# Kernel tuning notes

Measured on AMD Instinct MI355X. Metric: run time of the kernel, lower is better.

## Reference

```python
import jax, jax.numpy as jnp
import numpy as np

N = 16384          # batch of signals
DIM_T = 256        # time steps per signal
DT = 0.01          # integration dt (intg_lev=1 -> dt_intg = dt)
NUF = 256          # num_units_feat
HID_XI = 128       # hidlayers_xi
HID_AUX = 64       # hidlayers_aux1_dec
LEN_INTG = DIM_T   # (dim_t-1)*intg_lev + 1 with intg_lev=1


def _linear_init(key, fan_in, fan_out):
    # torch nn.Linear default: U(-1/sqrt(fan_in), 1/sqrt(fan_in))
    s = 1.0 / np.sqrt(fan_in)
    kw, kb = jax.random.split(key)
    W = jax.random.uniform(kw, (fan_in, fan_out), minval=-s, maxval=s, dtype=jnp.float32)
    b = jax.random.uniform(kb, (fan_out,), minval=-s, maxval=s, dtype=jnp.float32)
    return W, b


def setup_inputs() -> dict:
    key = jax.random.key(0)
    ks = jax.random.split(key, 12)
    data = jax.random.normal(ks[0], (N, DIM_T), dtype=jnp.float32)
    omega = jax.random.normal(ks[1], (N, 1), dtype=jnp.float32)
    eps = jax.random.normal(ks[2], (N, 1), dtype=jnp.float32)
    # feature extractor (mlp branch): [dim_t+1 -> 256 -> 256], relu after both (actfun_output=True)
    W_feat1, b_feat1 = _linear_init(ks[3], DIM_T + 1, NUF)
    W_feat2, b_feat2 = _linear_init(ks[4], NUF, NUF)
    # xi mean head: MLP [256 -> 128 -> 1] then Softplus
    W_xim1, b_xim1 = _linear_init(ks[5], NUF, HID_XI)
    W_xim2, b_xim2 = _linear_init(ks[6], HID_XI, 1)
    # xi lnvar head: MLP [256 -> 128 -> 1]
    W_xil1, b_xil1 = _linear_init(ks[7], NUF, HID_XI)
    W_xil2, b_xil2 = _linear_init(ks[8], HID_XI, 1)
    # decoder aux1 MLP: [dim_z_aux1+1=2 -> 64 -> 1]
    W_aux1, b_aux1 = _linear_init(ks[9], 2, HID_AUX)
    W_aux2, b_aux2 = _linear_init(ks[10], HID_AUX, 1)
    return dict(data=data, omega=omega, eps=eps,
                W_feat1=W_feat1, b_feat1=b_feat1, W_feat2=W_feat2, b_feat2=b_feat2,
                W_xim1=W_xim1, b_xim1=b_xim1, W_xim2=W_xim2, b_xim2=b_xim2,
                W_xil1=W_xil1, b_xil1=b_xil1, W_xil2=W_xil2, b_xil2=b_xil2,
                W_aux1=W_aux1, b_aux1=b_aux1, W_aux2=W_aux2, b_aux2=b_aux2)


def reference(data, omega, eps,
              W_feat1, b_feat1, W_feat2, b_feat2,
              W_xim1, b_xim1, W_xim2, b_xim2,
              W_xil1, b_xil1, W_xil2, b_xil2,
              W_aux1, b_aux1, W_aux2, b_aux2):
    relu = jax.nn.relu
    # ---- encode_xi ----
    x_ = jnp.concatenate([data, omega], axis=1)                 # [n, dim_t+1]
    feat = relu(relu(x_ @ W_feat1 + b_feat1) @ W_feat2 + b_feat2)  # [n, 256]
    xi_mean = jax.nn.softplus(relu(feat @ W_xim1 + b_xim1) @ W_xim2 + b_xim2)  # [n, 1]
    xi_lnvar = relu(feat @ W_xil1 + b_xil1) @ W_xil2 + b_xil2                  # [n, 1]
    # ---- draw (reparameterization + clamp to feasible range [0, 1]) ----
    xi = xi_mean + jnp.exp(0.5 * xi_lnvar) * eps
    xi = jnp.clip(xi, 0.0, 1.0)
    # ---- decode: Euler odeint over LEN_INTG steps of state yy=[y, dy/dt] ----
    init_y = data[:, :1]                                        # [n, 1]
    initcond = jnp.concatenate([init_y, jnp.zeros_like(init_y)], axis=1)  # [n, 2]

    def step(yy, _):
        # physics: d[y, v]/dt = [v, 0]; aux MLP adds acceleration from (z_aux1=omega, y)
        aux_in = jnp.concatenate([omega, yy[:, :1]], axis=1)    # [n, 2]
        acc = relu(aux_in @ W_aux1 + b_aux1) @ W_aux2 + b_aux2  # [n, 1]
        dyy = jnp.concatenate([yy[:, 1:2], acc], axis=1)        # [n, 2]
        return yy + DT * dyy, yy

    _, yy_seq = jax.lax.scan(step, initcond, None, length=LEN_INTG)  # [len_intg, n, 2]
    y_seq = yy_seq[:, :, 0].T                                   # [n, dim_t] (intg_lev=1)
    t_intg = DT * jnp.arange(LEN_INTG, dtype=jnp.float32)       # [dim_t]
    x_PAB = jnp.exp(-jnp.abs(xi) * t_intg[None, :]) * y_seq     # [n, dim_t]
    return xi_mean, xi_lnvar, x_PAB
```

## Files before the change

kernel.cpp:

```cpp
#include <hip/hip_runtime.h>
#include <math.h>

#define NROWS 16384
#define DT_C 0.01f

typedef short s16x8 __attribute__((ext_vector_type(8)));
typedef float f32x4 __attribute__((ext_vector_type(4)));
typedef float f32x2 __attribute__((ext_vector_type(2)));

__device__ __forceinline__ unsigned short f2bf(float f) {
    unsigned u = __float_as_uint(f);
    u += 0x7fffu + ((u >> 16) & 1u);
    return (unsigned short)(u >> 16);
}
__device__ __forceinline__ unsigned pack2bf(float a, float b) {
    return (unsigned)f2bf(a) | ((unsigned)f2bf(b) << 16);
}
template <int CTRL>
__device__ __forceinline__ float dppadd(float v) {
    int x = __builtin_amdgcn_update_dpp(0, __float_as_int(v), CTRL, 0xF, 0xF, true);
    return v + __int_as_float(x);
}
__device__ __forceinline__ float sum8(float p) {
    p = dppadd<0xB1>(p);
    p = dppadd<0x4E>(p);
    p = dppadd<0x141>(p);
    return p;
}

__global__ __launch_bounds__(256) void prep_k(
    const float* __restrict__ Wf1, const float* __restrict__ Wf2,
    const float* __restrict__ Wm1, const float* __restrict__ Wl1,
    const float* __restrict__ bm1, const float* __restrict__ bl1,
    unsigned short* __restrict__ wpack, float* __restrict__ biasH)
{
    const int id = blockIdx.x * 256 + threadIdx.x;
    const int n  = id & 255;
    const int k8 = (id >> 8) & 31;
    const int s  = id >> 13;

    unsigned short tmp[8];
    #pragma unroll
    for (int j = 0; j < 8; ++j) {
        const int k = k8 * 8 + j;
        float v;
        if (s == 0)      v = Wf1[k * 256 + n];
        else if (s == 1) v = Wf2[k * 256 + n];
        else             v = (n < 128) ? Wm1[k * 128 + n] : Wl1[k * 128 + n - 128];
        tmp[j] = f2bf(v);
    }
    *(uint4*)&wpack[((s * 32 + k8) * 256 + n) * 8] = *(const uint4*)tmp;

    if (id < 256) biasH[id] = (id < 128) ? bm1[id] : bl1[id - 128];
}

__global__ __launch_bounds__(256, 2) void fused_k(
    const float* __restrict__ data, const float* __restrict__ omega,
    const float* __restrict__ eps_g,
    const unsigned short* __restrict__ wpack, const float* __restrict__ biasH,
    const float* __restrict__ bf1, const float* __restrict__ bf2,
    const float* __restrict__ w256g,
    const float* __restrict__ Wm2, const float* __restrict__ bm2,
    const float* __restrict__ Wl2, const float* __restrict__ bl2,
    const float* __restrict__ Wa1, const float* __restrict__ ba1,
    const float* __restrict__ Wa2, const float* __restrict__ ba2,
    float* __restrict__ out_mean, float* __restrict__ out_lnvar,
    float* __restrict__ xout)
{
    __shared__ __align__(16) unsigned char smem[33024];
    unsigned short* As1 = (unsigned short*)smem;
    unsigned short* Hs  = (unsigned short*)(smem + 16384);
    float* headsF = (float*)smem;
    float* omg = (float*)(smem + 32768);
    float* xiS = omg + 32;

    const int tid  = threadIdx.x;
    const int wid  = tid >> 6;
    const int lane = tid & 63;
    const int ln   = lane & 15;
    const int quad = lane >> 4;
    const int r0   = blockIdx.x * 32;

    {
        #pragma unroll
        for (int g2 = 0; g2 < 8; ++g2) {
            const int unit = g2 * 256 + tid;
            const int m    = unit >> 6;
            const int c16  = unit & 63;
            const int kblk = c16 >> 1;
            const int h    = c16 & 1;
            const float4 v = *(const float4*)&data[(size_t)(r0 + m) * 256 + c16 * 4];
            unsigned* d = (unsigned*)&As1[((kblk * 32) + (m ^ (kblk & 7))) * 8 + h * 4];
            d[0] = pack2bf(v.x, v.y);
            d[1] = pack2bf(v.z, v.w);
        }
        if (tid < 32) omg[tid] = omega[r0 + tid];
    }
    __syncthreads();

    {
        const int r   = tid >> 3;
        const int l   = tid & 7;
        const int row = r0 + r;
        const float om = omg[r];
        const float pseed = ba2[0] * 0.125f;

        f32x2 w1v[4], Av[4], w2v[4];
        #pragma unroll
        for (int i = 0; i < 4; ++i) {
            const f32x2 w0 = *(const f32x2*)&Wa1[l * 8 + i * 2];
            const f32x2 bb = *(const f32x2*)&ba1[l * 8 + i * 2];
            w1v[i] = *(const f32x2*)&Wa1[64 + l * 8 + i * 2];
            w2v[i] = *(const f32x2*)&Wa2[l * 8 + i * 2];
            Av[i]  = f32x2{fmaf(om, w0.x, bb.x), fmaf(om, w0.y, bb.y)};
        }

        auto partial = [&](float y) -> float {
            const f32x2 y2 = f32x2{y, y};
            f32x2 acc2 = f32x2{pseed, 0.f};
            #pragma unroll
            for (int i = 0; i < 4; ++i) {
                f32x2 h = __builtin_elementwise_fma(y2, w1v[i], Av[i]);
                h = __builtin_elementwise_max(h, f32x2{0.f, 0.f});
                acc2 = __builtin_elementwise_fma(h, w2v[i], acc2);
            }
            return acc2.x + acc2.y;
        };

        const float y0 = data[(size_t)row * 256];
        float ym = y0;
        float yc = y0;
        const float DT2 = DT_C * DT_C;
        float pr = sum8(partial(ym));

        float* orow = xout + (size_t)row * 256 + l * 4;
        for (int tb = 0; tb < 8; ++tb) {
            float cur[4];
            #pragma unroll
            for (int j = 0; j < 32; ++j) {
                if ((j >> 2) == l) cur[j & 3] = ym;
                float pn = sum8(partial(yc));
                const float ynext = fmaf(DT2, pr, fmaf(2.f, yc, -ym));
                ym = yc; yc = ynext; pr = pn;
            }
            *(float4*)&orow[tb * 32] = *(const float4*)cur;
        }
    }

    f32x4 acc[2][4];

    auto seed = [&](const float* bias) {
        #pragma unroll
        for (int nt = 0; nt < 4; ++nt) {
            const float b = bias[wid * 64 + nt * 16 + ln];
            acc[0][nt] = f32x4{b, b, b, b};
            acc[1][nt] = acc[0][nt];
        }
    };

    auto run_stage = [&](const unsigned short* Ap, const unsigned short* wp) {
        #pragma unroll
        for (int c = 0; c < 4; ++c) {
            #pragma unroll
            for (int kk = 0; kk < 2; ++kk) {
                const int kb   = kk * 4 + quad;
                const int kblk = c * 8 + kb;
                const int f    = kblk & 7;
                s16x8 b0 = *(const s16x8*)&wp[((size_t)(kblk * 256) + wid * 64 + 0 * 16 + ln) * 8];
                s16x8 b1 = *(const s16x8*)&wp[((size_t)(kblk * 256) + wid * 64 + 1 * 16 + ln) * 8];
                s16x8 b2 = *(const s16x8*)&wp[((size_t)(kblk * 256) + wid * 64 + 2 * 16 + ln) * 8];
                s16x8 b3 = *(const s16x8*)&wp[((size_t)(kblk * 256) + wid * 64 + 3 * 16 + ln) * 8];
                s16x8 a0 = *(const s16x8*)&Ap[(kblk * 32 + (ln ^ f)) * 8];
                s16x8 a1 = *(const s16x8*)&Ap[(kblk * 32 + ((ln ^ f) + 16)) * 8];
                acc[0][0] = __builtin_amdgcn_mfma_f32_16x16x32_bf16(a0, b0, acc[0][0], 0, 0, 0);
                acc[1][0] = __builtin_amdgcn_mfma_f32_16x16x32_bf16(a1, b0, acc[1][0], 0, 0, 0);
                acc[0][1] = __builtin_amdgcn_mfma_f32_16x16x32_bf16(a0, b1, acc[0][1], 0, 0, 0);
                acc[1][1] = __builtin_amdgcn_mfma_f32_16x16x32_bf16(a1, b1, acc[1][1], 0, 0, 0);
                acc[0][2] = __builtin_amdgcn_mfma_f32_16x16x32_bf16(a0, b2, acc[0][2], 0, 0, 0);
                acc[1][2] = __builtin_amdgcn_mfma_f32_16x16x32_bf16(a1, b2, acc[1][2], 0, 0, 0);
                acc[0][3] = __builtin_amdgcn_mfma_f32_16x16x32_bf16(a0, b3, acc[0][3], 0, 0, 0);
                acc[1][3] = __builtin_amdgcn_mfma_f32_16x16x32_bf16(a1, b3, acc[1][3], 0, 0, 0);
            }
        }
    };

    auto write_packed = [&](unsigned short* dst, bool addOm) {
        #pragma unroll
        for (int nt = 0; nt < 4; ++nt) {
            const int col = wid * 64 + nt * 16 + ln;
            const int kg  = col >> 3, f = kg & 7, jj = col & 7;
            const float wo = addOm ? w256g[col] : 0.f;
            #pragma unroll
            for (int mt = 0; mt < 2; ++mt) {
                #pragma unroll
                for (int r = 0; r < 4; ++r) {
                    const int row = mt * 16 + quad * 4 + r;
                    float v = acc[mt][nt][r];
                    if (addOm) v = fmaf(omg[row], wo, v);
                    v = fmaxf(v, 0.f);
                    dst[(kg * 32 + (row ^ f)) * 8 + jj] = f2bf(v);
                }
            }
        }
    };

    seed(bf1);
    run_stage(As1, wpack);
    write_packed(Hs, true);
    __syncthreads();
    seed(bf2);
    run_stage(Hs, wpack + 65536);
    write_packed(As1, false);
    __syncthreads();
    seed(biasH);
    run_stage(As1, wpack + 131072);
    __syncthreads();
    #pragma unroll
    for (int nt = 0; nt < 4; ++nt) {
        const int col = wid * 64 + nt * 16 + ln;
        #pragma unroll
        for (int mt = 0; mt < 2; ++mt) {
            #pragma unroll
            for (int r = 0; r < 4; ++r) {
                const int row = mt * 16 + quad * 4 + r;
                headsF[row * 256 + ((col + row * 8) & 255)] = fmaxf(acc[mt][nt][r], 0.f);
            }
        }
    }
    __syncthreads();

    {
        const int m = tid >> 3, l = tid & 7;
        float pm = 0.f, pl = 0.f;
        #pragma unroll
        for (int q = 0; q < 4; ++q) {
            const int c0 = l * 16 + q * 4;
            const float4 hm = *(const float4*)&headsF[m * 256 + ((c0 + m * 8) & 255)];
            const float4 wm = *(const float4*)&Wm2[c0];
            const float4 hl = *(const float4*)&headsF[m * 256 + ((128 + c0 + m * 8) & 255)];
            const float4 wl = *(const float4*)&Wl2[c0];
            pm = fmaf(hm.w, wm.w, fmaf(hm.z, wm.z, fmaf(hm.y, wm.y, fmaf(hm.x, wm.x, pm))));
            pl = fmaf(hl.w, wl.w, fmaf(hl.z, wl.z, fmaf(hl.y, wl.y, fmaf(hl.x, wl.x, pl))));
        }
        pm = sum8(pm);
        pl = sum8(pl);
        if (l == 0) {
            const float xm  = pm + bm2[0];
            const float mean = fmaxf(xm, 0.f) + log1pf(expf(-fabsf(xm)));
            const float lnv  = pl + bl2[0];
            out_mean[r0 + m]  = mean;
            out_lnvar[r0 + m] = lnv;
            float xi = mean + expf(0.5f * lnv) * eps_g[r0 + m];
            xiS[m] = fminf(fmaxf(xi, 0.f), 1.f);
        }
    }
    __syncthreads();

    {
        const int r   = tid >> 3;
        const int l   = tid & 7;
        const float nxdt = -xiS[r] * DT_C;
        float* orow = xout + (size_t)(r0 + r) * 256 + l * 4;
        #pragma unroll
        for (int tb = 0; tb < 8; ++tb) {
            float4 v = *(const float4*)&orow[tb * 32];
            const int c0 = tb * 32 + l * 4;
            v.x *= __expf(nxdt * (float)(c0 + 0));
            v.y *= __expf(nxdt * (float)(c0 + 1));
            v.z *= __expf(nxdt * (float)(c0 + 2));
            v.w *= __expf(nxdt * (float)(c0 + 3));
            *(float4*)&orow[tb * 32] = v;
        }
    }
}

extern "C" void kernel_launch(void* const* d_in, const int* in_sizes, int n_in,
                              void* d_out, int out_size, void* d_ws, size_t ws_size,
                              hipStream_t stream)
{
    const float* data    = (const float*)d_in[0];
    const float* omega   = (const float*)d_in[1];
    const float* eps     = (const float*)d_in[2];
    const float* W_feat1 = (const float*)d_in[3];
    const float* b_feat1 = (const float*)d_in[4];
    const float* W_feat2 = (const float*)d_in[5];
    const float* b_feat2 = (const float*)d_in[6];
    const float* W_xim1  = (const float*)d_in[7];
    const float* b_xim1  = (const float*)d_in[8];
    const float* W_xim2  = (const float*)d_in[9];
    const float* b_xim2  = (const float*)d_in[10];
    const float* W_xil1  = (const float*)d_in[11];
    const float* b_xil1  = (const float*)d_in[12];
    const float* W_xil2  = (const float*)d_in[13];
    const float* b_xil2  = (const float*)d_in[14];
    const float* W_aux1  = (const float*)d_in[15];
    const float* b_aux1  = (const float*)d_in[16];
    const float* W_aux2  = (const float*)d_in[17];
    const float* b_aux2  = (const float*)d_in[18];

    float* out_mean  = (float*)d_out;
    float* out_lnvar = out_mean + NROWS;
    float* out_x     = out_lnvar + NROWS;

    unsigned short* wpack = (unsigned short*)d_ws;
    float* biasH = (float*)((char*)d_ws + 3 * 32 * 256 * 8 * 2);

    prep_k<<<96, 256, 0, stream>>>(W_feat1, W_feat2, W_xim1, W_xil1,
                                   b_xim1, b_xil1, wpack, biasH);
    fused_k<<<512, 256, 0, stream>>>(data, omega, eps, wpack, biasH,
                                     b_feat1, b_feat2, W_feat1 + 256 * 256,
                                     W_xim2, b_xim2, W_xil2, b_xil2,
                                     W_aux1, b_aux1, W_aux2, b_aux2,
                                     out_mean, out_lnvar, out_x);
}
```

Baseline: 141.1 us.

## Replace per-step aux MLP with piecewise-linear segment tracking over sorted ReLU breakpoints

The 64-unit ReLU aux MLP is a piecewise-linear function of y for a fixed omega. The new code precomputes the breakpoints -a/w per row, sorts them with a rank count in shared memory, and stores per-segment slope and intercept deltas. The Euler loop, run by one thread per row, then evaluates acc as segB*y+segA and walks across segments as y crosses breakpoints. It also fuses the exp(-xi t) decay into the integration loop, using a running multiplicative factor instead of a second read-modify-write pass. The cost is a serial loop in one thread of eight per row, more shared memory that may reduce occupancy, and edge-case handling for ties and w=0 breakpoints.

```diff
diff --git a/kernel.cpp b/kernel.cpp
--- a/kernel.cpp
+++ b/kernel.cpp
@@ -7,6 +7,8 @@
 typedef short s16x8 __attribute__((ext_vector_type(8)));
 typedef float f32x4 __attribute__((ext_vector_type(4)));
 typedef float f32x2 __attribute__((ext_vector_type(2)));
+typedef unsigned long long u64;
+typedef unsigned long long u64x2 __attribute__((ext_vector_type(2)));
 
 __device__ __forceinline__ unsigned short f2bf(float f) {
     unsigned u = __float_as_uint(f);
@@ -26,6 +28,10 @@
     p = dppadd<0x4E>(p);
     p = dppadd<0x141>(p);
     return p;
+}
+__device__ __forceinline__ unsigned ordf(float f) {
+    unsigned u = __float_as_uint(f);
+    return u ^ ((unsigned)((int)u >> 31) | 0x80000000u);
 }
 
 __global__ __launch_bounds__(256) void prep_k(
@@ -67,12 +73,15 @@
     float* __restrict__ out_mean, float* __restrict__ out_lnvar,
     float* __restrict__ xout)
 {
-    __shared__ __align__(16) unsigned char smem[33024];
+    __shared__ __align__(16) unsigned char smem[59136];
     unsigned short* As1 = (unsigned short*)smem;
     unsigned short* Hs  = (unsigned short*)(smem + 16384);
     float* headsF = (float*)smem;
     float* omg = (float*)(smem + 32768);
     float* xiS = omg + 32;
+    float* tS  = (float*)(smem + 33024);
+    float* dP  = (float*)(smem + 41728);
+    u64*  keyU = (u64*)(smem + 41728);
 
     const int tid  = threadIdx.x;
     const int wid  = tid >> 6;
@@ -96,54 +105,63 @@
         }
         if (tid < 32) omg[tid] = omega[r0 + tid];
     }
-    __syncthreads();
-
+
+    const int sr = tid >> 3;
+    const int sl = tid & 7;
+    float tA[8], dAv[8], dBv[8];
+    u64 key[8];
+    float k0f, Af, Bf, y0_s;
     {
-        const int r   = tid >> 3;
-        const int l   = tid & 7;
-        const int row = r0 + r;
-        const float om = omg[r];
-        const float pseed = ba2[0] * 0.125f;
-
-        f32x2 w1v[4], Av[4], w2v[4];
-        #pragma unroll
-        for (int i = 0; i < 4; ++i) {
-            const f32x2 w0 = *(const f32x2*)&Wa1[l * 8 + i * 2];
-            const f32x2 bb = *(const f32x2*)&ba1[l * 8 + i * 2];
-            w1v[i] = *(const f32x2*)&Wa1[64 + l * 8 + i * 2];
-            w2v[i] = *(const f32x2*)&Wa2[l * 8 + i * 2];
-            Av[i]  = f32x2{fmaf(om, w0.x, bb.x), fmaf(om, w0.y, bb.y)};
-        }
-
-        auto partial = [&](float y) -> float {
-            const f32x2 y2 = f32x2{y, y};
-            f32x2 acc2 = f32x2{pseed, 0.f};
+        const float om_s = omega[r0 + sr];
+        y0_s = data[(size_t)(r0 + sr) * 256];
+        const u64 ky0 = ((u64)ordf(y0_s)) << 6;
+        float k0p = 0.f, Ap = 0.f, Bp = 0.f;
+        #pragma unroll
+        for (int m = 0; m < 8; ++m) {
+            const int i = sl * 8 + m;
+            const float a = fmaf(om_s, Wa1[i], ba1[i]);
+            const float w = Wa1[64 + i];
+            const float c = Wa2[i];
+            const float ca = c * a, cw = c * w;
+            const bool wpos = w > 0.f;
+            tA[m]  = -a / w;
+            dAv[m] = wpos ? ca : -ca;
+            dBv[m] = wpos ? cw : -cw;
+            key[m] = (((u64)ordf(tA[m])) << 6) | (u64)i;
+            const bool crossed = key[m] < ky0;
+            if (wpos == crossed) { Ap += ca; Bp += cw; }
+            k0p += crossed ? 1.f : 0.f;
+            keyU[sr * 64 + i] = key[m];
+        }
+        k0f = sum8(k0p);
+        Af  = sum8(Ap) + ba2[0];
+        Bf  = sum8(Bp);
+    }
+    __syncthreads();
+
+    {
+        int rk[8] = {0, 0, 0, 0, 0, 0, 0, 0};
+        const u64* krow = keyU + sr * 64;
+        for (int j = 0; j < 64; j += 2) {
+            const u64x2 kk = *(const u64x2*)&krow[j];
             #pragma unroll
-            for (int i = 0; i < 4; ++i) {
-                f32x2 h = __builtin_elementwise_fma(y2, w1v[i], Av[i]);
-                h = __builtin_elementwise_max(h, f32x2{0.f, 0.f});
-                acc2 = __builtin_elementwise_fma(h, w2v[i], acc2);
-            }
-            return acc2.x + acc2.y;
-        };
-
-        const float y0 = data[(size_t)row * 256];
-        float ym = y0;
-        float yc = y0;
-        const float DT2 = DT_C * DT_C;
-        float pr = sum8(partial(ym));
-
-        float* orow = xout + (size_t)row * 256 + l * 4;
-        for (int tb = 0; tb < 8; ++tb) {
-            float cur[4];
-            #pragma unroll
-            for (int j = 0; j < 32; ++j) {
-                if ((j >> 2) == l) cur[j & 3] = ym;
-                float pn = sum8(partial(yc));
-                const float ynext = fmaf(DT2, pr, fmaf(2.f, yc, -ym));
-                ym = yc; yc = ynext; pr = pn;
-            }
-            *(float4*)&orow[tb * 32] = *(const float4*)cur;
+            for (int m = 0; m < 8; ++m)
+                rk[m] += (int)(kk.x < key[m]) + (int)(kk.y < key[m]);
+        }
+        __syncthreads();
+        #pragma unroll
+        for (int m = 0; m < 8; ++m) {
+            const int idx = sr * 68 + 2 + rk[m];
+            tS[idx] = tA[m];
+            *(f32x2*)&dP[2 * idx] = f32x2{dAv[m], dBv[m]};
+        }
+        if (sl == 0) {
+            const int b = sr * 68;
+            const float INFV = __builtin_inff();
+            tS[b] = -INFV; tS[b + 1] = -INFV; tS[b + 66] = INFV; tS[b + 67] = INFV;
+            const f32x2 z = {0.f, 0.f};
+            *(f32x2*)&dP[2 * b] = z;          *(f32x2*)&dP[2 * (b + 1)] = z;
+            *(f32x2*)&dP[2 * (b + 66)] = z;   *(f32x2*)&dP[2 * (b + 67)] = z;
         }
     }
 
@@ -256,20 +274,53 @@
     }
     __syncthreads();
 
-    {
-        const int r   = tid >> 3;
-        const int l   = tid & 7;
-        const float nxdt = -xiS[r] * DT_C;
-        float* orow = xout + (size_t)(r0 + r) * 256 + l * 4;
-        #pragma unroll
-        for (int tb = 0; tb < 8; ++tb) {
-            float4 v = *(const float4*)&orow[tb * 32];
-            const int c0 = tb * 32 + l * 4;
-            v.x *= __expf(nxdt * (float)(c0 + 0));
-            v.y *= __expf(nxdt * (float)(c0 + 1));
-            v.z *= __expf(nxdt * (float)(c0 + 2));
-            v.w *= __expf(nxdt * (float)(c0 + 3));
-            *(float4*)&orow[tb * 32] = v;
+    if (sl == 0) {
+        const float xi   = xiS[sr];
+        const float dfac = expf(-xi * DT_C);
+        const float* tSr = tS + sr * 68 + 2;
+        const float* dPb = dP + (sr * 68 + 2) * 2;
+        int   k    = (int)k0f;
+        float segA = Af, segB = Bf;
+        float tLo  = tSr[k - 1], tHi = tSr[k], tHi2 = tSr[k + 1], tLo2 = tSr[k - 2];
+        f32x2 dU = *(const f32x2*)&dPb[2 * k];
+        f32x2 dD = *(const f32x2*)&dPb[2 * (k - 1)];
+        float ym = y0_s, yc = y0_s;
+        float pr = fmaf(segB, y0_s, segA);
+        float d  = 1.f;
+        const float DT2 = DT_C * DT_C;
+        float* orow = xout + (size_t)(r0 + sr) * 256;
+
+        auto step = [&](float& dst) {
+            if (__builtin_expect(yc >= tHi, 0)) {
+                do {
+                    segA += dU.x; segB += dU.y;
+                    dD = dU;
+                    tLo2 = tLo; tLo = tHi; tHi = tHi2;
+                    ++k;
+                    tHi2 = tSr[k + 1];
+                    dU = *(const f32x2*)&dPb[2 * k];
+                } while (yc >= tHi);
+            } else if (__builtin_expect(yc < tLo, 0)) {
+                do {
+                    segA -= dD.x; segB -= dD.y;
+                    dU = dD;
+                    tHi2 = tHi; tHi = tLo; tLo = tLo2;
+                    --k;
+                    tLo2 = tSr[k - 2];
+                    dD = *(const f32x2*)&dPb[2 * (k - 1)];
+                } while (yc < tLo);
+            }
+            const float pn = fmaf(segB, yc, segA);
+            dst = ym * d;
+            d *= dfac;
+            const float yn = fmaf(DT2, pr, fmaf(2.f, yc, -ym));
+            ym = yc; yc = yn; pr = pn;
+        };
+
+        for (int g = 0; g < 64; ++g) {
+            float4 cv;
+            step(cv.x); step(cv.y); step(cv.z); step(cv.w);
+            *(float4*)&orow[g * 4] = cv;
         }
     }
 }
```

After: 147.6 us. 4.6% more time.

## Warp-specialize fused kernel: run ODE integration concurrently with MLP encoder

Applied to the files above, without the earlier changes.

Doubles the block to 512 threads. Four new wavefronts run the serial Euler ODE recurrence while the original four wavefronts run the MFMA encoder stages, so the latency-bound scan overlaps with the GEMMs instead of running before them. Block-wide barriers are replaced by LDS atomic counters with spin-waits among the four compute waves, plus a final wait for the ODE waves before the exp-decay scaling. Risks include spin-wait overhead, fewer registers per thread under launch_bounds(512,4), and the correctness hazards of hand-rolled synchronization.

```diff
diff --git a/kernel.cpp b/kernel.cpp
--- a/kernel.cpp
+++ b/kernel.cpp
@@ -54,7 +54,7 @@
     if (id < 256) biasH[id] = (id < 128) ? bm1[id] : bl1[id - 128];
 }
 
-__global__ __launch_bounds__(256, 2) void fused_k(
+__global__ __launch_bounds__(512, 4) void fused_k(
     const float* __restrict__ data, const float* __restrict__ omega,
     const float* __restrict__ eps_g,
     const unsigned short* __restrict__ wpack, const float* __restrict__ biasH,
@@ -68,6 +68,7 @@
     float* __restrict__ xout)
 {
     __shared__ __align__(16) unsigned char smem[33024];
+    __shared__ int syncc[8];
     unsigned short* As1 = (unsigned short*)smem;
     unsigned short* Hs  = (unsigned short*)(smem + 16384);
     float* headsF = (float*)smem;
@@ -80,6 +81,70 @@
     const int ln   = lane & 15;
     const int quad = lane >> 4;
     const int r0   = blockIdx.x * 32;
+
+    if (tid < 8) syncc[tid] = 0;
+    __syncthreads();
+
+    if (wid >= 4) {
+        const int st  = tid - 256;
+        const int r   = st >> 3;
+        const int l   = st & 7;
+        const int row = r0 + r;
+        const float om = omega[row];
+        const float pseed = ba2[0] * 0.125f;
+
+        f32x2 w1v[4], Av[4], w2v[4];
+        #pragma unroll
+        for (int i = 0; i < 4; ++i) {
+            const f32x2 w0 = *(const f32x2*)&Wa1[l * 8 + i * 2];
+            const f32x2 bb = *(const f32x2*)&ba1[l * 8 + i * 2];
+            w1v[i] = *(const f32x2*)&Wa1[64 + l * 8 + i * 2];
+            w2v[i] = *(const f32x2*)&Wa2[l * 8 + i * 2];
+            Av[i]  = f32x2{fmaf(om, w0.x, bb.x), fmaf(om, w0.y, bb.y)};
+        }
+
+        auto partial = [&](float y) -> float {
+            const f32x2 y2 = f32x2{y, y};
+            f32x2 acc2 = f32x2{pseed, 0.f};
+            #pragma unroll
+            for (int i = 0; i < 4; ++i) {
+                f32x2 h = __builtin_elementwise_fma(y2, w1v[i], Av[i]);
+                h = __builtin_elementwise_max(h, f32x2{0.f, 0.f});
+                acc2 = __builtin_elementwise_fma(h, w2v[i], acc2);
+            }
+            return acc2.x + acc2.y;
+        };
+
+        const float y0 = data[(size_t)row * 256];
+        float ym = y0;
+        float yc = y0;
+        const float DT2 = DT_C * DT_C;
+        float pr = sum8(partial(ym));
+
+        float* orow = xout + (size_t)row * 256 + l * 4;
+        for (int tb = 0; tb < 8; ++tb) {
+            float cur[4];
+            #pragma unroll
+            for (int j = 0; j < 32; ++j) {
+                if ((j >> 2) == l) cur[j & 3] = ym;
+                float pn = sum8(partial(yc));
+                const float ynext = fmaf(DT2, pr, fmaf(2.f, yc, -ym));
+                ym = yc; yc = ynext; pr = pn;
+            }
+            *(float4*)&orow[tb * 32] = *(const float4*)cur;
+        }
+
+        __threadfence_block();
+        if (lane == 0) atomicAdd(&syncc[6], 1);
+        return;
+    }
+
+    auto fsync = [&](int slot) {
+        __threadfence_block();
+        if (lane == 0) atomicAdd(&syncc[slot], 1);
+        while (*(volatile int*)&syncc[slot] < 4) __builtin_amdgcn_s_sleep(2);
+        __threadfence_block();
+    };
 
     {
         #pragma unroll
@@ -96,56 +161,7 @@
         }
         if (tid < 32) omg[tid] = omega[r0 + tid];
     }
-    __syncthreads();
-
-    {
-        const int r   = tid >> 3;
-        const int l   = tid & 7;
-        const int row = r0 + r;
-        const float om = omg[r];
-        const float pseed = ba2[0] * 0.125f;
-
-        f32x2 w1v[4], Av[4], w2v[4];
-        #pragma unroll
-        for (int i = 0; i < 4; ++i) {
-            const f32x2 w0 = *(const f32x2*)&Wa1[l * 8 + i * 2];
-            const f32x2 bb = *(const f32x2*)&ba1[l * 8 + i * 2];
-            w1v[i] = *(const f32x2*)&Wa1[64 + l * 8 + i * 2];
-            w2v[i] = *(const f32x2*)&Wa2[l * 8 + i * 2];
-            Av[i]  = f32x2{fmaf(om, w0.x, bb.x), fmaf(om, w0.y, bb.y)};
-        }
-
-        auto partial = [&](float y) -> float {
-            const f32x2 y2 = f32x2{y, y};
-            f32x2 acc2 = f32x2{pseed, 0.f};
-            #pragma unroll
-            for (int i = 0; i < 4; ++i) {
-                f32x2 h = __builtin_elementwise_fma(y2, w1v[i], Av[i]);
-                h = __builtin_elementwise_max(h, f32x2{0.f, 0.f});
-                acc2 = __builtin_elementwise_fma(h, w2v[i], acc2);
-            }
-            return acc2.x + acc2.y;
-        };
-
-        const float y0 = data[(size_t)row * 256];
-        float ym = y0;
-        float yc = y0;
-        const float DT2 = DT_C * DT_C;
-        float pr = sum8(partial(ym));
-
-        float* orow = xout + (size_t)row * 256 + l * 4;
-        for (int tb = 0; tb < 8; ++tb) {
-            float cur[4];
-            #pragma unroll
-            for (int j = 0; j < 32; ++j) {
-                if ((j >> 2) == l) cur[j & 3] = ym;
-                float pn = sum8(partial(yc));
-                const float ynext = fmaf(DT2, pr, fmaf(2.f, yc, -ym));
-                ym = yc; yc = ynext; pr = pn;
-            }
-            *(float4*)&orow[tb * 32] = *(const float4*)cur;
-        }
-    }
+    fsync(0);
 
     f32x4 acc[2][4];
 
@@ -207,14 +223,14 @@
     seed(bf1);
     run_stage(As1, wpack);
     write_packed(Hs, true);
-    __syncthreads();
+    fsync(1);
     seed(bf2);
     run_stage(Hs, wpack + 65536);
     write_packed(As1, false);
-    __syncthreads();
+    fsync(2);
     seed(biasH);
     run_stage(As1, wpack + 131072);
-    __syncthreads();
+    fsync(3);
     #pragma unroll
     for (int nt = 0; nt < 4; ++nt) {
         const int col = wid * 64 + nt * 16 + ln;
@@ -227,7 +243,7 @@
             }
         }
     }
-    __syncthreads();
+    fsync(4);
 
     {
         const int m = tid >> 3, l = tid & 7;
@@ -254,7 +270,10 @@
             xiS[m] = fminf(fmaxf(xi, 0.f), 1.f);
         }
     }
-    __syncthreads();
+    fsync(5);
+
+    while (*(volatile int*)&syncc[6] < 4) __builtin_amdgcn_s_sleep(2);
+    __threadfence_block();
 
     {
         const int r   = tid >> 3;
@@ -307,7 +326,7 @@
 
     prep_k<<<96, 256, 0, stream>>>(W_feat1, W_feat2, W_xim1, W_xil1,
                                    b_xim1, b_xil1, wpack, biasH);
-    fused_k<<<512, 256, 0, stream>>>(data, omega, eps, wpack, biasH,
+    fused_k<<<512, 512, 0, stream>>>(data, omega, eps, wpack, biasH,
                                      b_feat1, b_feat2, W_feat1 + 256 * 256,
                                      W_xim2, b_xim2, W_xil2, b_xil2,
                                      W_aux1, b_aux1, W_aux2, b_aux2,
```

After: 142.0 us. No clear change (+0.7%).

## Split serial ODE scan into its own kernel before MFMA encoder kernel

Applied to the files above, without the earlier changes.

Moves the Euler scan of the aux MLP out of the fused kernel into a separate scan_k launch that writes raw trajectories to the output. The MFMA encoder kernel then loads those raw trajectories into registers at its start and applies the exponential decay once xi is known. The aim is to shorten the fused kernel's critical path and remove the latency-bound scan from it, possibly freeing registers. In exchange it adds a launch, and the trajectory buffer now makes an extra round trip through global memory between the two kernels.

```diff
diff --git a/kernel.cpp b/kernel.cpp
--- a/kernel.cpp
+++ b/kernel.cpp
@@ -54,7 +54,61 @@
     if (id < 256) biasH[id] = (id < 128) ? bm1[id] : bl1[id - 128];
 }
 
-__global__ __launch_bounds__(256, 2) void fused_k(
+__global__ __launch_bounds__(256) void scan_k(
+    const float* __restrict__ data, const float* __restrict__ omega,
+    const float* __restrict__ Wa1, const float* __restrict__ ba1,
+    const float* __restrict__ Wa2, const float* __restrict__ ba2,
+    float* __restrict__ xout)
+{
+    const int tid = threadIdx.x;
+    const int row = blockIdx.x * 32 + (tid >> 3);
+    const int l   = tid & 7;
+    const float om = omega[row];
+    const float pseed = ba2[0] * 0.125f;
+
+    f32x2 w1v[4], Av[4], w2v[4];
+    #pragma unroll
+    for (int i = 0; i < 4; ++i) {
+        const f32x2 w0 = *(const f32x2*)&Wa1[l * 8 + i * 2];
+        const f32x2 bb = *(const f32x2*)&ba1[l * 8 + i * 2];
+        w1v[i] = *(const f32x2*)&Wa1[64 + l * 8 + i * 2];
+        w2v[i] = *(const f32x2*)&Wa2[l * 8 + i * 2];
+        Av[i]  = f32x2{fmaf(om, w0.x, bb.x), fmaf(om, w0.y, bb.y)};
+    }
+
+    auto partial = [&](float y) -> float {
+        const f32x2 y2 = f32x2{y, y};
+        f32x2 acc2 = f32x2{pseed, 0.f};
+        #pragma unroll
+        for (int i = 0; i < 4; ++i) {
+            f32x2 h = __builtin_elementwise_fma(y2, w1v[i], Av[i]);
+            h = __builtin_elementwise_max(h, f32x2{0.f, 0.f});
+            acc2 = __builtin_elementwise_fma(h, w2v[i], acc2);
+        }
+        return acc2.x + acc2.y;
+    };
+
+    const float y0 = data[(size_t)row * 256];
+    float ym = y0;
+    float yc = y0;
+    const float DT2 = DT_C * DT_C;
+    float pr = sum8(partial(ym));
+
+    float* orow = xout + (size_t)row * 256 + l * 4;
+    for (int tb = 0; tb < 8; ++tb) {
+        float cur[4];
+        #pragma unroll
+        for (int j = 0; j < 32; ++j) {
+            if ((j >> 2) == l) cur[j & 3] = ym;
+            float pn = sum8(partial(yc));
+            const float ynext = fmaf(DT2, pr, fmaf(2.f, yc, -ym));
+            ym = yc; yc = ynext; pr = pn;
+        }
+        *(float4*)&orow[tb * 32] = *(const float4*)cur;
+    }
+}
+
+__global__ __launch_bounds__(256, 2) void mfma_decay_k(
     const float* __restrict__ data, const float* __restrict__ omega,
     const float* __restrict__ eps_g,
     const unsigned short* __restrict__ wpack, const float* __restrict__ biasH,
@@ -62,8 +116,6 @@
     const float* __restrict__ w256g,
     const float* __restrict__ Wm2, const float* __restrict__ bm2,
     const float* __restrict__ Wl2, const float* __restrict__ bl2,
-    const float* __restrict__ Wa1, const float* __restrict__ ba1,
-    const float* __restrict__ Wa2, const float* __restrict__ ba2,
     float* __restrict__ out_mean, float* __restrict__ out_lnvar,
     float* __restrict__ xout)
 {
@@ -80,6 +132,13 @@
     const int ln   = lane & 15;
     const int quad = lane >> 4;
     const int r0   = blockIdx.x * 32;
+
+    const int er = tid >> 3;
+    const int el = tid & 7;
+    float* erow = xout + (size_t)(r0 + er) * 256 + el * 4;
+    float4 rawv[8];
+    #pragma unroll
+    for (int tb = 0; tb < 8; ++tb) rawv[tb] = *(const float4*)&erow[tb * 32];
 
     {
         #pragma unroll
@@ -97,55 +156,6 @@
         if (tid < 32) omg[tid] = omega[r0 + tid];
     }
     __syncthreads();
-
-    {
-        const int r   = tid >> 3;
-        const int l   = tid & 7;
-        const int row = r0 + r;
-        const float om = omg[r];
-        const float pseed = ba2[0] * 0.125f;
-
-        f32x2 w1v[4], Av[4], w2v[4];
-        #pragma unroll
-        for (int i = 0; i < 4; ++i) {
-            const f32x2 w0 = *(const f32x2*)&Wa1[l * 8 + i * 2];
-            const f32x2 bb = *(const f32x2*)&ba1[l * 8 + i * 2];
-            w1v[i] = *(const f32x2*)&Wa1[64 + l * 8 + i * 2];
-            w2v[i] = *(const f32x2*)&Wa2[l * 8 + i * 2];
-            Av[i]  = f32x2{fmaf(om, w0.x, bb.x), fmaf(om, w0.y, bb.y)};
-        }
-
-        auto partial = [&](float y) -> float {
-            const f32x2 y2 = f32x2{y, y};
-            f32x2 acc2 = f32x2{pseed, 0.f};
-            #pragma unroll
-            for (int i = 0; i < 4; ++i) {
-                f32x2 h = __builtin_elementwise_fma(y2, w1v[i], Av[i]);
-                h = __builtin_elementwise_max(h, f32x2{0.f, 0.f});
-                acc2 = __builtin_elementwise_fma(h, w2v[i], acc2);
-            }
-            return acc2.x + acc2.y;
-        };
-
-        const float y0 = data[(size_t)row * 256];
-        float ym = y0;
-        float yc = y0;
-        const float DT2 = DT_C * DT_C;
-        float pr = sum8(partial(ym));
-
-        float* orow = xout + (size_t)row * 256 + l * 4;
-        for (int tb = 0; tb < 8; ++tb) {
-            float cur[4];
-            #pragma unroll
-            for (int j = 0; j < 32; ++j) {
-                if ((j >> 2) == l) cur[j & 3] = ym;
-                float pn = sum8(partial(yc));
-                const float ynext = fmaf(DT2, pr, fmaf(2.f, yc, -ym));
-                ym = yc; yc = ynext; pr = pn;
-            }
-            *(float4*)&orow[tb * 32] = *(const float4*)cur;
-        }
-    }
 
     f32x4 acc[2][4];
 
@@ -257,19 +267,16 @@
     __syncthreads();
 
     {
-        const int r   = tid >> 3;
-        const int l   = tid & 7;
-        const float nxdt = -xiS[r] * DT_C;
-        float* orow = xout + (size_t)(r0 + r) * 256 + l * 4;
+        const float nxdt = -xiS[er] * DT_C;
         #pragma unroll
         for (int tb = 0; tb < 8; ++tb) {
-            float4 v = *(const float4*)&orow[tb * 32];
-            const int c0 = tb * 32 + l * 4;
+            float4 v = rawv[tb];
+            const int c0 = tb * 32 + el * 4;
             v.x *= __expf(nxdt * (float)(c0 + 0));
             v.y *= __expf(nxdt * (float)(c0 + 1));
             v.z *= __expf(nxdt * (float)(c0 + 2));
             v.w *= __expf(nxdt * (float)(c0 + 3));
-            *(float4*)&orow[tb * 32] = v;
+            *(float4*)&erow[tb * 32] = v;
         }
     }
 }
@@ -307,9 +314,10 @@
 
     prep_k<<<96, 256, 0, stream>>>(W_feat1, W_feat2, W_xim1, W_xil1,
                                    b_xim1, b_xil1, wpack, biasH);
-    fused_k<<<512, 256, 0, stream>>>(data, omega, eps, wpack, biasH,
-                                     b_feat1, b_feat2, W_feat1 + 256 * 256,
-                                     W_xim2, b_xim2, W_xil2, b_xil2,
-                                     W_aux1, b_aux1, W_aux2, b_aux2,
-                                     out_mean, out_lnvar, out_x);
-}
+    scan_k<<<512, 256, 0, stream>>>(data, omega, W_aux1, b_aux1, W_aux2, b_aux2,
+                                    out_x);
+    mfma_decay_k<<<512, 256, 0, stream>>>(data, omega, eps, wpack, biasH,
+                                          b_feat1, b_feat2, W_feat1 + 256 * 256,
+                                          W_xim2, b_xim2, W_xil2, b_xil2,
+                                          out_mean, out_lnvar, out_x);
+}
```

Result: slower. 150.1 us (+6.4%).
